# Kernel optimization log

Measured on AMD Instinct MI355X. Metric: run time of the kernel, lower is better.

The kernel has to match this reference:

```python
import jax, jax.numpy as jnp
import numpy as np

B, NQ, NKV = 4, 2048, 2048
D_MODEL, N_HEADS, D_K = 1024, 16, 64


def setup_inputs() -> dict:
    key = jax.random.key(0)
    ks = jax.random.split(key, 7)
    s = 1.0 / np.sqrt(D_MODEL)
    return {
        "x": jax.random.normal(ks[0], (B, NQ, D_MODEL), jnp.float32),
        "encoding": jax.random.normal(ks[1], (B, NKV, D_MODEL), jnp.float32),
        "position_bias": jax.random.normal(ks[2], (1, N_HEADS, NQ, NKV), jnp.float32),
        "Wq": jax.random.normal(ks[3], (D_MODEL, D_MODEL), jnp.float32) * s,
        "Wk": jax.random.normal(ks[4], (D_MODEL, D_MODEL), jnp.float32) * s,
        "Wv": jax.random.normal(ks[5], (D_MODEL, D_MODEL), jnp.float32) * s,
        "Wo": jax.random.normal(ks[6], (D_MODEL, D_MODEL), jnp.float32) * s,
    }


def _split_heads(t):
    b, n, _ = t.shape
    return t.reshape(b, n, N_HEADS, D_K).transpose(0, 2, 1, 3)


def reference(x, encoding, position_bias, Wq, Wk, Wv, Wo):
    # Projections (flax Dense, no bias): y = x @ kernel
    Q = _split_heads(x @ Wq)            # [B,H,NQ,Dk]
    K = _split_heads(encoding @ Wk)     # [B,H,NKV,Dk]
    V = _split_heads(encoding @ Wv)     # [B,H,NKV,Dk]
    # T5-style: NO 1/sqrt(d_k) scaling; additive position bias before softmax
    scores = jnp.einsum('bhqd,bhkd->bhqk', Q, K) + position_bias
    attn = jax.nn.softmax(scores, axis=-1)
    ctx = jnp.einsum('bhqk,bhkd->bhqd', attn, V)    # [B,H,NQ,Dk]
    ctx = ctx.transpose(0, 2, 1, 3).reshape(x.shape[0], x.shape[1], D_MODEL)
    return ctx @ Wo
```

## Files before the change

### kernel.cpp

```cpp
#include <hip/hip_runtime.h>

#define B_   4
#define NQ_  2048
#define NKV_ 2048
#define H_   16
#define DK_  64
#define DM_  1024
#define DKV_ 2048

typedef _Float16 f16x8 __attribute__((ext_vector_type(8)));
typedef _Float16 f16x4 __attribute__((ext_vector_type(4)));
typedef float    f32x4 __attribute__((ext_vector_type(4)));

__device__ __forceinline__ void gload_lds16(const void* g, void* l) {
  __builtin_amdgcn_global_load_lds(
      (const __attribute__((address_space(1))) unsigned int*)g,
      (__attribute__((address_space(3))) unsigned int*)l, 16, 0, 0);
}

__global__ __launch_bounds__(256) void cast_f16(const float* __restrict__ in,
                                                _Float16* __restrict__ out, int n4) {
  int i = blockIdx.x * 256 + threadIdx.x;
  if (i >= n4) return;
  float4 v = ((const float4*)in)[i];
  f16x4 o = {(_Float16)v.x, (_Float16)v.y, (_Float16)v.z, (_Float16)v.w};
  *(f16x4*)(out + (size_t)i * 4) = o;
}

__global__ __launch_bounds__(256) void wtrans(const float* __restrict__ W,
                                              _Float16* __restrict__ Wt) {
  __shared__ float tile[32][33];
  int bx = blockIdx.x & 31, by = blockIdx.x >> 5;
  int tx = threadIdx.x & 31, ty = threadIdx.x >> 5;
#pragma unroll
  for (int j = 0; j < 4; ++j)
    tile[ty + j * 8][tx] = W[(size_t)(by * 32 + ty + j * 8) * 1024 + bx * 32 + tx];
  __syncthreads();
#pragma unroll
  for (int j = 0; j < 4; ++j)
    Wt[(size_t)(bx * 32 + ty + j * 8) * 1024 + by * 32 + tx] = (_Float16)tile[tx][ty + j * 8];
}

template <int F32OUT>
__global__ __launch_bounds__(256, 2) void gemm_bt(const _Float16* __restrict__ A,
                                                  const _Float16* __restrict__ Bt,
                                                  void* __restrict__ Cp,
                                                  int M, int N, int K) {
  __shared__ _Float16 As[128 * 32];
  __shared__ _Float16 Bs[128 * 32];
  const int nbn = N >> 7;
  const int bm = blockIdx.x / nbn, bn = blockIdx.x % nbn;
  const int t = threadIdx.x, w = t >> 6, l = t & 63;
  const int lr = l & 15, lg = l >> 4;
  const int wr = w >> 1, wc = w & 1;
  const int m0 = bm << 7, n0 = bn << 7;

  f32x4 acc[4][4] = {};

  for (int k0 = 0; k0 < K; k0 += 32) {
#pragma unroll
    for (int p = 0; p < 2; ++p) {
      int off = p * 4096 + w * 1024 + l * 16;
      int row = off >> 6;
      int col = (off & 63) >> 1;
      gload_lds16(A  + (size_t)(m0 + row) * K + k0 + col, (char*)As + p * 4096 + w * 1024);
      gload_lds16(Bt + (size_t)(n0 + row) * K + k0 + col, (char*)Bs + p * 4096 + w * 1024);
    }
    __syncthreads();
    f16x8 af[4], bq[4];
#pragma unroll
    for (int i = 0; i < 4; ++i) {
      af[i] = *(const f16x8*)((const char*)As + (wr * 64 + i * 16 + lr) * 64 + lg * 16);
      bq[i] = *(const f16x8*)((const char*)Bs + (wc * 64 + i * 16 + lr) * 64 + lg * 16);
    }
#pragma unroll
    for (int i = 0; i < 4; ++i)
#pragma unroll
      for (int j = 0; j < 4; ++j)
        acc[i][j] = __builtin_amdgcn_mfma_f32_16x16x32_f16(af[i], bq[j], acc[i][j], 0, 0, 0);
    __syncthreads();
  }
#pragma unroll
  for (int i = 0; i < 4; ++i)
#pragma unroll
    for (int j = 0; j < 4; ++j)
#pragma unroll
      for (int r = 0; r < 4; ++r) {
        size_t row = m0 + wr * 64 + i * 16 + lg * 4 + r;
        size_t col = n0 + wc * 64 + j * 16 + lr;
        if (F32OUT) ((float*)Cp)[row * N + col] = acc[i][j][r];
        else ((_Float16*)Cp)[row * N + col] = (_Float16)acc[i][j][r];
      }
}

__global__ __launch_bounds__(256) void vtrans(const _Float16* __restrict__ KVb,
                                              _Float16* __restrict__ Vt) {
  __shared__ _Float16 tile[64][72];
  int idx = blockIdx.x;
  int kt = idx & 31, h = (idx >> 5) & 15, b = idx >> 9;
  int kv0 = kt << 6;
  int t = threadIdx.x;
#pragma unroll
  for (int p = 0; p < 2; ++p) {
    int c = t + p * 256;
    int row = c >> 3, cb = (c & 7) * 16;
    f16x8 v = *(const f16x8*)(KVb + (size_t)(b * NKV_ + kv0 + row) * DKV_ + 1024 + h * 64 + cb / 2);
    *(f16x8*)((char*)&tile[row][0] + cb) = v;
  }
  __syncthreads();
  int d = t & 63, j0 = (t >> 6) * 2;
#pragma unroll
  for (int jj = 0; jj < 2; ++jj) {
    int kvs = (j0 + jj) * 8;
    f16x8 o;
#pragma unroll
    for (int u = 0; u < 8; ++u) o[u] = tile[kvs + u][d];
    *(f16x8*)(Vt + ((size_t)((b * H_ + h) * 64 + d)) * NKV_ + kv0 + kvs) = o;
  }
}

__global__ __launch_bounds__(256, 4) void attn(const _Float16* __restrict__ Qb,
                                               const _Float16* __restrict__ KVb,
                                               const _Float16* __restrict__ Vt,
                                               const float* __restrict__ bias,
                                               _Float16* __restrict__ ctx) {
  __shared__ _Float16 Ks[64 * 64];
  __shared__ _Float16 Vs[64 * 64];
  __shared__ _Float16 Ps[4][16 * 64];
  const float LOG2E = 1.44269504f;
  int idx = blockIdx.x;
  int b = idx & 3, qt = (idx >> 2) & 31, h = idx >> 7;
  int t = threadIdx.x, w = t >> 6, l = t & 63, lr = l & 15, lg = l >> 4;
  int qw = (qt << 6) + (w << 4);

  const _Float16* qp = Qb + (size_t)(b * NQ_ + qw + lr) * DM_ + h * 64 + lg * 8;
  f16x8 aq0 = *(const f16x8*)qp;
  f16x8 aq1 = *(const f16x8*)(qp + 32);
#pragma unroll
  for (int u = 0; u < 8; ++u) { aq0[u] = aq0[u] * (_Float16)LOG2E; aq1[u] = aq1[u] * (_Float16)LOG2E; }

  f32x4 acc[4] = {};
  float mrow = -1e30f;
  float lsum = 0.f;

  const _Float16* Kbase = KVb + (size_t)b * NKV_ * DKV_ + h * 64;
  const _Float16* Vtb   = Vt + (size_t)(b * H_ + h) * 64 * NKV_;
  const float*    biasq = bias + ((size_t)h * NQ_ + qw + lr) * NKV_ + lg * 4;

  const int srow = t >> 3;
  const int scb  = (t & 7) * 16;

  f16x8 kreg[2], vreg[2];

  auto LOADKV = [&](int kv0) {
#pragma unroll
    for (int p = 0; p < 2; ++p) {
      int row = srow + p * 32;
      kreg[p] = *(const f16x8*)(Kbase + (size_t)(kv0 + row) * DKV_ + scb / 2);
      vreg[p] = *(const f16x8*)(Vtb + (size_t)row * NKV_ + kv0 + scb / 2);
    }
  };

  LOADKV(0);

  for (int it = 0; it < 32; ++it) {
    const int kv0 = it << 6;

#pragma unroll
    for (int p = 0; p < 2; ++p) {
      int row = srow + p * 32;
      int off = (row * 128 + scb) ^ ((row & 7) << 4);
      *(f16x8*)((char*)Ks + off) = kreg[p];
      *(f16x8*)((char*)Vs + off) = vreg[p];
    }
    __syncthreads();

    const int kvn = (it < 31) ? kv0 + 64 : kv0;
    LOADKV(kvn);

    float4 bv4[4];
#pragma unroll
    for (int nt = 0; nt < 4; ++nt)
      bv4[nt] = *(const float4*)(biasq + kv0 + nt * 16);

    f32x4 s[4];
    __builtin_amdgcn_s_setprio(1);
#pragma unroll
    for (int nt = 0; nt < 4; ++nt) {
      int row = nt * 16 + lr;
      int sw = (row & 7) << 4;
      f16x8 kf0 = *(const f16x8*)((char*)Ks + ((row * 128 + lg * 16) ^ sw));
      f16x8 kf1 = *(const f16x8*)((char*)Ks + ((row * 128 + 64 + lg * 16) ^ sw));
      f32x4 z = {0.f, 0.f, 0.f, 0.f};
      z = __builtin_amdgcn_mfma_f32_16x16x32_f16(kf0, aq0, z, 0, 0, 0);
      s[nt] = __builtin_amdgcn_mfma_f32_16x16x32_f16(kf1, aq1, z, 0, 0, 0);
    }
    __builtin_amdgcn_s_setprio(0);

#pragma unroll
    for (int nt = 0; nt < 4; ++nt) {
      s[nt][0] = fmaf(bv4[nt].x, LOG2E, s[nt][0]);
      s[nt][1] = fmaf(bv4[nt].y, LOG2E, s[nt][1]);
      s[nt][2] = fmaf(bv4[nt].z, LOG2E, s[nt][2]);
      s[nt][3] = fmaf(bv4[nt].w, LOG2E, s[nt][3]);
    }

    float pmax = fmaxf(fmaxf(s[0][0], s[0][1]), fmaxf(s[0][2], s[0][3]));
#pragma unroll
    for (int nt = 1; nt < 4; ++nt)
      pmax = fmaxf(pmax, fmaxf(fmaxf(s[nt][0], s[nt][1]), fmaxf(s[nt][2], s[nt][3])));
    pmax = fmaxf(pmax, __shfl_xor(pmax, 16));
    pmax = fmaxf(pmax, __shfl_xor(pmax, 32));

    if (__any(pmax > mrow + 8.0f)) {
      float mn = fmaxf(mrow, pmax);
      float corr = exp2f(mrow - mn);
      mrow = mn;
      lsum *= corr;
#pragma unroll
      for (int nt = 0; nt < 4; ++nt)
#pragma unroll
        for (int r = 0; r < 4; ++r) acc[nt][r] *= corr;
    }

    float rs = 0.f;
#pragma unroll
    for (int nt = 0; nt < 4; ++nt)
#pragma unroll
      for (int r = 0; r < 4; ++r) {
        float p = exp2f(s[nt][r] - mrow);
        s[nt][r] = p;
        rs += p;
      }
    rs += __shfl_xor(rs, 16);
    rs += __shfl_xor(rs, 32);
    lsum += rs;

#pragma unroll
    for (int nt = 0; nt < 4; ++nt) {
      f16x4 pk = {(_Float16)s[nt][0], (_Float16)s[nt][1],
                  (_Float16)s[nt][2], (_Float16)s[nt][3]};
      int off = (lr * 128 + nt * 32 + lg * 8) ^ ((lr & 7) << 4);
      *(f16x4*)((char*)Ps[w] + off) = pk;
    }

    __builtin_amdgcn_s_setprio(1);
#pragma unroll
    for (int kk = 0; kk < 2; ++kk) {
      f16x8 pb = *(const f16x8*)((char*)Ps[w] +
                 ((lr * 128 + kk * 64 + lg * 16) ^ ((lr & 7) << 4)));
#pragma unroll
      for (int nt = 0; nt < 4; ++nt) {
        int row = nt * 16 + lr;
        f16x8 vf = *(const f16x8*)((char*)Vs +
                 ((row * 128 + kk * 64 + lg * 16) ^ ((row & 7) << 4)));
        acc[nt] = __builtin_amdgcn_mfma_f32_16x16x32_f16(vf, pb, acc[nt], 0, 0, 0);
      }
    }
    __builtin_amdgcn_s_setprio(0);
    __syncthreads();
  }

  float inv = 1.0f / lsum;
#pragma unroll
  for (int nt = 0; nt < 4; ++nt) {
    f16x4 o = {(_Float16)(acc[nt][0] * inv), (_Float16)(acc[nt][1] * inv),
               (_Float16)(acc[nt][2] * inv), (_Float16)(acc[nt][3] * inv)};
    *(f16x4*)(ctx + ((size_t)b * NQ_ + qw + lr) * DM_ + h * 64 + nt * 16 + lg * 4) = o;
  }
}

extern "C" void kernel_launch(void* const* d_in, const int* in_sizes, int n_in,
                              void* d_out, int out_size, void* d_ws, size_t ws_size,
                              hipStream_t stream) {
  const float* x    = (const float*)d_in[0];
  const float* enc  = (const float*)d_in[1];
  const float* bias = (const float*)d_in[2];
  const float* Wq   = (const float*)d_in[3];
  const float* Wk   = (const float*)d_in[4];
  const float* Wv   = (const float*)d_in[5];
  const float* Wo   = (const float*)d_in[6];
  char* ws = (char*)d_ws;
  const size_t MiB = 1024 * 1024;
  _Float16* WqT   = (_Float16*)(ws + 0 * MiB);
  _Float16* WkT   = (_Float16*)(ws + 2 * MiB);
  _Float16* WvT   = (_Float16*)(ws + 4 * MiB);
  _Float16* WoT   = (_Float16*)(ws + 6 * MiB);
  _Float16* xf    = (_Float16*)(ws + 8 * MiB);
  _Float16* encf  = (_Float16*)(ws + 24 * MiB);
  _Float16* Qb    = (_Float16*)(ws + 40 * MiB);
  _Float16* KVb   = (_Float16*)(ws + 56 * MiB);
  _Float16* Vt    = (_Float16*)(ws + 88 * MiB);
  _Float16* ctxf  = (_Float16*)(ws + 104 * MiB);

  wtrans<<<1024, 256, 0, stream>>>(Wq, WqT);
  wtrans<<<1024, 256, 0, stream>>>(Wk, WkT);
  wtrans<<<1024, 256, 0, stream>>>(Wv, WvT);
  wtrans<<<1024, 256, 0, stream>>>(Wo, WoT);
  cast_f16<<<8192, 256, 0, stream>>>(x, xf, 2097152);
  cast_f16<<<8192, 256, 0, stream>>>(enc, encf, 2097152);
  gemm_bt<0><<<512, 256, 0, stream>>>(xf, WqT, Qb, 8192, 1024, 1024);
  gemm_bt<0><<<1024, 256, 0, stream>>>(encf, WkT, KVb, 8192, 2048, 1024);
  vtrans<<<2048, 256, 0, stream>>>(KVb, Vt);
  attn<<<2048, 256, 0, stream>>>(Qb, KVb, Vt, bias, ctxf);
  gemm_bt<1><<<512, 256, 0, stream>>>(ctxf, WoT, d_out, 8192, 1024, 1024);
}
```

Before: 353.1 us.

## Switch attention to 32x32x16 MFMA with register-resident P via permlane swaps

The attention kernel moves from 16x16x32 to 32x32x16 MFMA tiles. Each wave now handles 32 query rows instead of 16, so each block covers 128 queries and the grid is halved. The softmax probabilities are packed to f16 and rearranged in registers with permlane32_swap, which replaces the round trip through the per-wave LDS P buffer. The aim is to reuse each K/V tile across twice as many queries and to cut LDS traffic. In exchange, register pressure per wave rises and the smaller grid gives fewer blocks to spread across the GPU.

```diff
diff --git a/kernel.cpp b/kernel.cpp
--- a/kernel.cpp
+++ b/kernel.cpp
@@ -10,7 +10,11 @@
 
 typedef _Float16 f16x8 __attribute__((ext_vector_type(8)));
 typedef _Float16 f16x4 __attribute__((ext_vector_type(4)));
+typedef _Float16 f16x2 __attribute__((ext_vector_type(2)));
 typedef float    f32x4 __attribute__((ext_vector_type(4)));
+typedef float    f32x16 __attribute__((ext_vector_type(16)));
+typedef unsigned u32x2 __attribute__((ext_vector_type(2)));
+typedef unsigned u32x4 __attribute__((ext_vector_type(4)));
 
 __device__ __forceinline__ void gload_lds16(const void* g, void* l) {
   __builtin_amdgcn_global_load_lds(
@@ -119,6 +123,12 @@
   }
 }
 
+__device__ __forceinline__ void plswap(unsigned& a, unsigned& b) {
+  u32x2 r = __builtin_amdgcn_permlane32_swap(a, b, false, false);
+  a = r[0];
+  b = r[1];
+}
+
 __global__ __launch_bounds__(256, 4) void attn(const _Float16* __restrict__ Qb,
                                                const _Float16* __restrict__ KVb,
                                                const _Float16* __restrict__ Vt,
@@ -126,26 +136,30 @@
                                                _Float16* __restrict__ ctx) {
   __shared__ _Float16 Ks[64 * 64];
   __shared__ _Float16 Vs[64 * 64];
-  __shared__ _Float16 Ps[4][16 * 64];
   const float LOG2E = 1.44269504f;
   int idx = blockIdx.x;
-  int b = idx & 3, qt = (idx >> 2) & 31, h = idx >> 7;
-  int t = threadIdx.x, w = t >> 6, l = t & 63, lr = l & 15, lg = l >> 4;
-  int qw = (qt << 6) + (w << 4);
-
-  const _Float16* qp = Qb + (size_t)(b * NQ_ + qw + lr) * DM_ + h * 64 + lg * 8;
-  f16x8 aq0 = *(const f16x8*)qp;
-  f16x8 aq1 = *(const f16x8*)(qp + 32);
-#pragma unroll
-  for (int u = 0; u < 8; ++u) { aq0[u] = aq0[u] * (_Float16)LOG2E; aq1[u] = aq1[u] * (_Float16)LOG2E; }
-
-  f32x4 acc[4] = {};
-  float mrow = -1e30f;
-  float lsum = 0.f;
-
-  const _Float16* Kbase = KVb + (size_t)b * NKV_ * DKV_ + h * 64;
-  const _Float16* Vtb   = Vt + (size_t)(b * H_ + h) * 64 * NKV_;
-  const float*    biasq = bias + ((size_t)h * NQ_ + qw + lr) * NKV_ + lg * 4;
+  int b = idx & 3, qt = (idx >> 2) & 15, hd = idx >> 6;
+  int t = threadIdx.x, w = t >> 6, l = t & 63;
+  int lq = l & 31, h = l >> 5;
+  int qw = (qt << 7) + (w << 5);
+
+  f16x8 qf[4];
+  {
+    const _Float16* qp = Qb + ((size_t)(b * NQ_ + qw + lq)) * DM_ + hd * 64 + h * 8;
+#pragma unroll
+    for (int ks = 0; ks < 4; ++ks) {
+      qf[ks] = *(const f16x8*)(qp + ks * 16);
+#pragma unroll
+      for (int u = 0; u < 8; ++u) qf[ks][u] = qf[ks][u] * (_Float16)LOG2E;
+    }
+  }
+
+  f32x16 acc[2] = {};
+  float mrow = -1e30f, lsum = 0.f;
+
+  const _Float16* Kbase = KVb + (size_t)b * NKV_ * DKV_ + hd * 64;
+  const _Float16* Vtb   = Vt + (size_t)(b * H_ + hd) * 64 * NKV_;
+  const float*    biasrow = bias + ((size_t)hd * NQ_ + qw + lq) * NKV_ + 4 * h;
 
   const int srow = t >> 3;
   const int scb  = (t & 7) * 16;
@@ -175,99 +189,98 @@
     }
     __syncthreads();
 
-    const int kvn = (it < 31) ? kv0 + 64 : kv0;
-    LOADKV(kvn);
-
-    float4 bv4[4];
-#pragma unroll
-    for (int nt = 0; nt < 4; ++nt)
-      bv4[nt] = *(const float4*)(biasq + kv0 + nt * 16);
-
-    f32x4 s[4];
-    __builtin_amdgcn_s_setprio(1);
-#pragma unroll
-    for (int nt = 0; nt < 4; ++nt) {
-      int row = nt * 16 + lr;
-      int sw = (row & 7) << 4;
-      f16x8 kf0 = *(const f16x8*)((char*)Ks + ((row * 128 + lg * 16) ^ sw));
-      f16x8 kf1 = *(const f16x8*)((char*)Ks + ((row * 128 + 64 + lg * 16) ^ sw));
-      f32x4 z = {0.f, 0.f, 0.f, 0.f};
-      z = __builtin_amdgcn_mfma_f32_16x16x32_f16(kf0, aq0, z, 0, 0, 0);
-      s[nt] = __builtin_amdgcn_mfma_f32_16x16x32_f16(kf1, aq1, z, 0, 0, 0);
-    }
-    __builtin_amdgcn_s_setprio(0);
-
-#pragma unroll
-    for (int nt = 0; nt < 4; ++nt) {
-      s[nt][0] = fmaf(bv4[nt].x, LOG2E, s[nt][0]);
-      s[nt][1] = fmaf(bv4[nt].y, LOG2E, s[nt][1]);
-      s[nt][2] = fmaf(bv4[nt].z, LOG2E, s[nt][2]);
-      s[nt][3] = fmaf(bv4[nt].w, LOG2E, s[nt][3]);
-    }
-
-    float pmax = fmaxf(fmaxf(s[0][0], s[0][1]), fmaxf(s[0][2], s[0][3]));
-#pragma unroll
-    for (int nt = 1; nt < 4; ++nt)
-      pmax = fmaxf(pmax, fmaxf(fmaxf(s[nt][0], s[nt][1]), fmaxf(s[nt][2], s[nt][3])));
-    pmax = fmaxf(pmax, __shfl_xor(pmax, 16));
-    pmax = fmaxf(pmax, __shfl_xor(pmax, 32));
-
-    if (__any(pmax > mrow + 8.0f)) {
-      float mn = fmaxf(mrow, pmax);
-      float corr = exp2f(mrow - mn);
-      mrow = mn;
-      lsum *= corr;
-#pragma unroll
-      for (int nt = 0; nt < 4; ++nt)
-#pragma unroll
-        for (int r = 0; r < 4; ++r) acc[nt][r] *= corr;
-    }
-
-    float rs = 0.f;
-#pragma unroll
-    for (int nt = 0; nt < 4; ++nt)
-#pragma unroll
-      for (int r = 0; r < 4; ++r) {
-        float p = exp2f(s[nt][r] - mrow);
-        s[nt][r] = p;
+    LOADKV((it < 31) ? kv0 + 64 : kv0);
+
+#pragma unroll
+    for (int T = 0; T < 2; ++T) {
+      const float* bp = biasrow + kv0 + 32 * T;
+      float4 bv[4];
+#pragma unroll
+      for (int g = 0; g < 4; ++g) bv[g] = *(const float4*)(bp + 8 * g);
+
+      f32x16 s = {};
+      const int krow = 32 * T + lq;
+      const int ksw = (krow & 7) << 4;
+      __builtin_amdgcn_s_setprio(1);
+#pragma unroll
+      for (int ks = 0; ks < 4; ++ks) {
+        f16x8 kf = *(const f16x8*)((char*)Ks + ((krow * 128 + ks * 32 + h * 16) ^ ksw));
+        s = __builtin_amdgcn_mfma_f32_32x32x16_f16(kf, qf[ks], s, 0, 0, 0);
+      }
+      __builtin_amdgcn_s_setprio(0);
+
+#pragma unroll
+      for (int g = 0; g < 4; ++g) {
+        s[4 * g + 0] = fmaf(bv[g].x, LOG2E, s[4 * g + 0]);
+        s[4 * g + 1] = fmaf(bv[g].y, LOG2E, s[4 * g + 1]);
+        s[4 * g + 2] = fmaf(bv[g].z, LOG2E, s[4 * g + 2]);
+        s[4 * g + 3] = fmaf(bv[g].w, LOG2E, s[4 * g + 3]);
+      }
+
+      float pmax = s[0];
+#pragma unroll
+      for (int r = 1; r < 16; ++r) pmax = fmaxf(pmax, s[r]);
+      pmax = fmaxf(pmax, __shfl_xor(pmax, 32));
+
+      if (__any(pmax > mrow + 8.0f)) {
+        float mn = fmaxf(mrow, pmax);
+        float corr = exp2f(mrow - mn);
+        mrow = mn;
+        lsum *= corr;
+#pragma unroll
+        for (int r = 0; r < 16; ++r) { acc[0][r] *= corr; acc[1][r] *= corr; }
+      }
+
+      float rs = 0.f;
+#pragma unroll
+      for (int r = 0; r < 16; ++r) {
+        float p = exp2f(s[r] - mrow);
+        s[r] = p;
         rs += p;
       }
-    rs += __shfl_xor(rs, 16);
-    rs += __shfl_xor(rs, 32);
-    lsum += rs;
-
-#pragma unroll
-    for (int nt = 0; nt < 4; ++nt) {
-      f16x4 pk = {(_Float16)s[nt][0], (_Float16)s[nt][1],
-                  (_Float16)s[nt][2], (_Float16)s[nt][3]};
-      int off = (lr * 128 + nt * 32 + lg * 8) ^ ((lr & 7) << 4);
-      *(f16x4*)((char*)Ps[w] + off) = pk;
-    }
-
-    __builtin_amdgcn_s_setprio(1);
-#pragma unroll
-    for (int kk = 0; kk < 2; ++kk) {
-      f16x8 pb = *(const f16x8*)((char*)Ps[w] +
-                 ((lr * 128 + kk * 64 + lg * 16) ^ ((lr & 7) << 4)));
-#pragma unroll
-      for (int nt = 0; nt < 4; ++nt) {
-        int row = nt * 16 + lr;
-        f16x8 vf = *(const f16x8*)((char*)Vs +
-                 ((row * 128 + kk * 64 + lg * 16) ^ ((row & 7) << 4)));
-        acc[nt] = __builtin_amdgcn_mfma_f32_16x16x32_f16(vf, pb, acc[nt], 0, 0, 0);
-      }
-    }
-    __builtin_amdgcn_s_setprio(0);
+      rs += __shfl_xor(rs, 32);
+      lsum += rs;
+
+      unsigned dw[4][2];
+#pragma unroll
+      for (int g = 0; g < 4; ++g)
+#pragma unroll
+        for (int j = 0; j < 2; ++j)
+          dw[g][j] = __builtin_bit_cast(unsigned,
+              __builtin_amdgcn_cvt_pkrtz(s[4 * g + 2 * j], s[4 * g + 2 * j + 1]));
+
+      __builtin_amdgcn_s_setprio(1);
+#pragma unroll
+      for (int kp = 0; kp < 2; ++kp) {
+        unsigned A0 = dw[2 * kp][0], B0 = dw[2 * kp + 1][0];
+        unsigned A1 = dw[2 * kp][1], B1 = dw[2 * kp + 1][1];
+        plswap(A0, B0);
+        plswap(A1, B1);
+        u32x4 pv4 = {A0, A1, B0, B1};
+        f16x8 pf = __builtin_bit_cast(f16x8, pv4);
+        const int kvs = (2 * T + kp) * 32 + h * 16;
+#pragma unroll
+        for (int dt = 0; dt < 2; ++dt) {
+          int vrow = 32 * dt + lq;
+          f16x8 vf = *(const f16x8*)((char*)Vs + ((vrow * 128 + kvs) ^ ((vrow & 7) << 4)));
+          acc[dt] = __builtin_amdgcn_mfma_f32_32x32x16_f16(vf, pf, acc[dt], 0, 0, 0);
+        }
+      }
+      __builtin_amdgcn_s_setprio(0);
+    }
     __syncthreads();
   }
 
   float inv = 1.0f / lsum;
-#pragma unroll
-  for (int nt = 0; nt < 4; ++nt) {
-    f16x4 o = {(_Float16)(acc[nt][0] * inv), (_Float16)(acc[nt][1] * inv),
-               (_Float16)(acc[nt][2] * inv), (_Float16)(acc[nt][3] * inv)};
-    *(f16x4*)(ctx + ((size_t)b * NQ_ + qw + lr) * DM_ + h * 64 + nt * 16 + lg * 4) = o;
-  }
+  _Float16* cp = ctx + ((size_t)b * NQ_ + qw + lq) * DM_ + hd * 64 + 4 * h;
+#pragma unroll
+  for (int dt = 0; dt < 2; ++dt)
+#pragma unroll
+    for (int g = 0; g < 4; ++g) {
+      f16x4 o = {(_Float16)(acc[dt][4 * g + 0] * inv), (_Float16)(acc[dt][4 * g + 1] * inv),
+                 (_Float16)(acc[dt][4 * g + 2] * inv), (_Float16)(acc[dt][4 * g + 3] * inv)};
+      *(f16x4*)(cp + 32 * dt + 8 * g) = o;
+    }
 }
 
 extern "C" void kernel_launch(void* const* d_in, const int* in_sizes, int n_in,
@@ -302,6 +315,6 @@
   gemm_bt<0><<<512, 256, 0, stream>>>(xf, WqT, Qb, 8192, 1024, 1024);
   gemm_bt<0><<<1024, 256, 0, stream>>>(encf, WkT, KVb, 8192, 2048, 1024);
   vtrans<<<2048, 256, 0, stream>>>(KVb, Vt);
-  attn<<<2048, 256, 0, stream>>>(Qb, KVb, Vt, bias, ctxf);
+  attn<<<1024, 256, 0, stream>>>(Qb, KVb, Vt, bias, ctxf);
   gemm_bt<1><<<512, 256, 0, stream>>>(ctxf, WoT, d_out, 8192, 1024, 1024);
 }
```

Result: slower. 378.7 us (+7.3%).

## Stage 128-wide KV tiles per sync and remap block indices for L2 locality

Applied to the files above, without the earlier changes.

The attention kernel now stages 128 KV rows per iteration, split into two 64-wide softmax sub-steps, which halves the number of barriers and global-to-LDS rounds. The V tile layout and swizzle change to a 256-byte row stride to match. Block indices are also remapped so that eight consecutive blocks share the same batch and neighbouring head/query-tile pairs, aiming to improve cache reuse of K/V across concurrently running blocks. LDS usage doubles for K and V and more registers hold prefetched tiles, which may lower occupancy.

```diff
diff --git a/kernel.cpp b/kernel.cpp
--- a/kernel.cpp
+++ b/kernel.cpp
@@ -124,16 +124,19 @@
                                                const _Float16* __restrict__ Vt,
                                                const float* __restrict__ bias,
                                                _Float16* __restrict__ ctx) {
-  __shared__ _Float16 Ks[64 * 64];
-  __shared__ _Float16 Vs[64 * 64];
+  __shared__ _Float16 Ks[128 * 64];
+  __shared__ _Float16 Vs[64 * 128];
   __shared__ _Float16 Ps[4][16 * 64];
   const float LOG2E = 1.44269504f;
   int idx = blockIdx.x;
-  int b = idx & 3, qt = (idx >> 2) & 31, h = idx >> 7;
+  int xr = idx & 7, m = idx >> 3;
+  int b = m & 3;
+  int hq = (m >> 2) * 8 + xr;
+  int hd = hq >> 5, qt = hq & 31;
   int t = threadIdx.x, w = t >> 6, l = t & 63, lr = l & 15, lg = l >> 4;
   int qw = (qt << 6) + (w << 4);
 
-  const _Float16* qp = Qb + (size_t)(b * NQ_ + qw + lr) * DM_ + h * 64 + lg * 8;
+  const _Float16* qp = Qb + (size_t)(b * NQ_ + qw + lr) * DM_ + hd * 64 + lg * 8;
   f16x8 aq0 = *(const f16x8*)qp;
   f16x8 aq1 = *(const f16x8*)(qp + 32);
 #pragma unroll
@@ -143,121 +146,124 @@
   float mrow = -1e30f;
   float lsum = 0.f;
 
-  const _Float16* Kbase = KVb + (size_t)b * NKV_ * DKV_ + h * 64;
-  const _Float16* Vtb   = Vt + (size_t)(b * H_ + h) * 64 * NKV_;
-  const float*    biasq = bias + ((size_t)h * NQ_ + qw + lr) * NKV_ + lg * 4;
-
-  const int srow = t >> 3;
-  const int scb  = (t & 7) * 16;
-
-  f16x8 kreg[2], vreg[2];
+  const _Float16* Kbase = KVb + (size_t)b * NKV_ * DKV_ + hd * 64;
+  const _Float16* Vtb   = Vt + (size_t)(b * H_ + hd) * 64 * NKV_;
+  const float*    biasq = bias + ((size_t)hd * NQ_ + qw + lr) * NKV_ + lg * 4;
+
+  const int ksrow = t >> 3, kscb = (t & 7) * 16;
+  const int vsrow = t >> 4, vscb = (t & 15) * 16;
+
+  f16x8 kreg[4], vreg[4];
 
   auto LOADKV = [&](int kv0) {
 #pragma unroll
-    for (int p = 0; p < 2; ++p) {
-      int row = srow + p * 32;
-      kreg[p] = *(const f16x8*)(Kbase + (size_t)(kv0 + row) * DKV_ + scb / 2);
-      vreg[p] = *(const f16x8*)(Vtb + (size_t)row * NKV_ + kv0 + scb / 2);
+    for (int p = 0; p < 4; ++p) {
+      kreg[p] = *(const f16x8*)(Kbase + (size_t)(kv0 + ksrow + p * 32) * DKV_ + kscb / 2);
+      vreg[p] = *(const f16x8*)(Vtb + (size_t)(vsrow + p * 16) * NKV_ + kv0 + vscb / 2);
     }
   };
 
   LOADKV(0);
 
-  for (int it = 0; it < 32; ++it) {
-    const int kv0 = it << 6;
-
-#pragma unroll
-    for (int p = 0; p < 2; ++p) {
-      int row = srow + p * 32;
-      int off = (row * 128 + scb) ^ ((row & 7) << 4);
-      *(f16x8*)((char*)Ks + off) = kreg[p];
-      *(f16x8*)((char*)Vs + off) = vreg[p];
+  for (int it = 0; it < 16; ++it) {
+    const int kv0 = it << 7;
+
+#pragma unroll
+    for (int p = 0; p < 4; ++p) {
+      int krow = ksrow + p * 32;
+      *(f16x8*)((char*)Ks + ((krow * 128 + kscb) ^ ((krow & 7) << 4))) = kreg[p];
+      int vrow = vsrow + p * 16;
+      *(f16x8*)((char*)Vs + ((vrow * 256 + vscb) ^ ((vrow & 15) << 4))) = vreg[p];
     }
     __syncthreads();
 
-    const int kvn = (it < 31) ? kv0 + 64 : kv0;
-    LOADKV(kvn);
-
-    float4 bv4[4];
-#pragma unroll
-    for (int nt = 0; nt < 4; ++nt)
-      bv4[nt] = *(const float4*)(biasq + kv0 + nt * 16);
-
-    f32x4 s[4];
-    __builtin_amdgcn_s_setprio(1);
-#pragma unroll
-    for (int nt = 0; nt < 4; ++nt) {
-      int row = nt * 16 + lr;
-      int sw = (row & 7) << 4;
-      f16x8 kf0 = *(const f16x8*)((char*)Ks + ((row * 128 + lg * 16) ^ sw));
-      f16x8 kf1 = *(const f16x8*)((char*)Ks + ((row * 128 + 64 + lg * 16) ^ sw));
-      f32x4 z = {0.f, 0.f, 0.f, 0.f};
-      z = __builtin_amdgcn_mfma_f32_16x16x32_f16(kf0, aq0, z, 0, 0, 0);
-      s[nt] = __builtin_amdgcn_mfma_f32_16x16x32_f16(kf1, aq1, z, 0, 0, 0);
-    }
-    __builtin_amdgcn_s_setprio(0);
-
-#pragma unroll
-    for (int nt = 0; nt < 4; ++nt) {
-      s[nt][0] = fmaf(bv4[nt].x, LOG2E, s[nt][0]);
-      s[nt][1] = fmaf(bv4[nt].y, LOG2E, s[nt][1]);
-      s[nt][2] = fmaf(bv4[nt].z, LOG2E, s[nt][2]);
-      s[nt][3] = fmaf(bv4[nt].w, LOG2E, s[nt][3]);
-    }
-
-    float pmax = fmaxf(fmaxf(s[0][0], s[0][1]), fmaxf(s[0][2], s[0][3]));
-#pragma unroll
-    for (int nt = 1; nt < 4; ++nt)
-      pmax = fmaxf(pmax, fmaxf(fmaxf(s[nt][0], s[nt][1]), fmaxf(s[nt][2], s[nt][3])));
-    pmax = fmaxf(pmax, __shfl_xor(pmax, 16));
-    pmax = fmaxf(pmax, __shfl_xor(pmax, 32));
-
-    if (__any(pmax > mrow + 8.0f)) {
-      float mn = fmaxf(mrow, pmax);
-      float corr = exp2f(mrow - mn);
-      mrow = mn;
-      lsum *= corr;
+    LOADKV((it < 15) ? kv0 + 128 : kv0);
+
+#pragma unroll
+    for (int T = 0; T < 2; ++T) {
+      const int kvh = kv0 + 64 * T;
+
+      float4 bv4[4];
 #pragma unroll
       for (int nt = 0; nt < 4; ++nt)
-#pragma unroll
-        for (int r = 0; r < 4; ++r) acc[nt][r] *= corr;
-    }
-
-    float rs = 0.f;
-#pragma unroll
-    for (int nt = 0; nt < 4; ++nt)
-#pragma unroll
-      for (int r = 0; r < 4; ++r) {
-        float p = exp2f(s[nt][r] - mrow);
-        s[nt][r] = p;
-        rs += p;
-      }
-    rs += __shfl_xor(rs, 16);
-    rs += __shfl_xor(rs, 32);
-    lsum += rs;
-
-#pragma unroll
-    for (int nt = 0; nt < 4; ++nt) {
-      f16x4 pk = {(_Float16)s[nt][0], (_Float16)s[nt][1],
-                  (_Float16)s[nt][2], (_Float16)s[nt][3]};
-      int off = (lr * 128 + nt * 32 + lg * 8) ^ ((lr & 7) << 4);
-      *(f16x4*)((char*)Ps[w] + off) = pk;
-    }
-
-    __builtin_amdgcn_s_setprio(1);
-#pragma unroll
-    for (int kk = 0; kk < 2; ++kk) {
-      f16x8 pb = *(const f16x8*)((char*)Ps[w] +
-                 ((lr * 128 + kk * 64 + lg * 16) ^ ((lr & 7) << 4)));
+        bv4[nt] = *(const float4*)(biasq + kvh + nt * 16);
+
+      f32x4 s[4];
+      __builtin_amdgcn_s_setprio(1);
 #pragma unroll
       for (int nt = 0; nt < 4; ++nt) {
-        int row = nt * 16 + lr;
-        f16x8 vf = *(const f16x8*)((char*)Vs +
-                 ((row * 128 + kk * 64 + lg * 16) ^ ((row & 7) << 4)));
-        acc[nt] = __builtin_amdgcn_mfma_f32_16x16x32_f16(vf, pb, acc[nt], 0, 0, 0);
-      }
-    }
-    __builtin_amdgcn_s_setprio(0);
+        int row = T * 64 + nt * 16 + lr;
+        int sw = (row & 7) << 4;
+        f16x8 kf0 = *(const f16x8*)((char*)Ks + ((row * 128 + lg * 16) ^ sw));
+        f16x8 kf1 = *(const f16x8*)((char*)Ks + ((row * 128 + 64 + lg * 16) ^ sw));
+        f32x4 z = {0.f, 0.f, 0.f, 0.f};
+        z = __builtin_amdgcn_mfma_f32_16x16x32_f16(kf0, aq0, z, 0, 0, 0);
+        s[nt] = __builtin_amdgcn_mfma_f32_16x16x32_f16(kf1, aq1, z, 0, 0, 0);
+      }
+      __builtin_amdgcn_s_setprio(0);
+
+#pragma unroll
+      for (int nt = 0; nt < 4; ++nt) {
+        s[nt][0] = fmaf(bv4[nt].x, LOG2E, s[nt][0]);
+        s[nt][1] = fmaf(bv4[nt].y, LOG2E, s[nt][1]);
+        s[nt][2] = fmaf(bv4[nt].z, LOG2E, s[nt][2]);
+        s[nt][3] = fmaf(bv4[nt].w, LOG2E, s[nt][3]);
+      }
+
+      float pmax = fmaxf(fmaxf(s[0][0], s[0][1]), fmaxf(s[0][2], s[0][3]));
+#pragma unroll
+      for (int nt = 1; nt < 4; ++nt)
+        pmax = fmaxf(pmax, fmaxf(fmaxf(s[nt][0], s[nt][1]), fmaxf(s[nt][2], s[nt][3])));
+      pmax = fmaxf(pmax, __shfl_xor(pmax, 16));
+      pmax = fmaxf(pmax, __shfl_xor(pmax, 32));
+
+      if (__any(pmax > mrow + 8.0f)) {
+        float mn = fmaxf(mrow, pmax);
+        float corr = exp2f(mrow - mn);
+        mrow = mn;
+        lsum *= corr;
+#pragma unroll
+        for (int nt = 0; nt < 4; ++nt)
+#pragma unroll
+          for (int r = 0; r < 4; ++r) acc[nt][r] *= corr;
+      }
+
+      float rs = 0.f;
+#pragma unroll
+      for (int nt = 0; nt < 4; ++nt)
+#pragma unroll
+        for (int r = 0; r < 4; ++r) {
+          float p = exp2f(s[nt][r] - mrow);
+          s[nt][r] = p;
+          rs += p;
+        }
+      rs += __shfl_xor(rs, 16);
+      rs += __shfl_xor(rs, 32);
+      lsum += rs;
+
+#pragma unroll
+      for (int nt = 0; nt < 4; ++nt) {
+        f16x4 pk = {(_Float16)s[nt][0], (_Float16)s[nt][1],
+                    (_Float16)s[nt][2], (_Float16)s[nt][3]};
+        int off = (lr * 128 + nt * 32 + lg * 8) ^ ((lr & 7) << 4);
+        *(f16x4*)((char*)Ps[w] + off) = pk;
+      }
+
+      __builtin_amdgcn_s_setprio(1);
+#pragma unroll
+      for (int kk = 0; kk < 2; ++kk) {
+        f16x8 pb = *(const f16x8*)((char*)Ps[w] +
+                   ((lr * 128 + kk * 64 + lg * 16) ^ ((lr & 7) << 4)));
+#pragma unroll
+        for (int nt = 0; nt < 4; ++nt) {
+          int vrow = nt * 16 + lr;
+          f16x8 vf = *(const f16x8*)((char*)Vs +
+                   ((vrow * 256 + T * 128 + kk * 64 + lg * 16) ^ ((vrow & 15) << 4)));
+          acc[nt] = __builtin_amdgcn_mfma_f32_16x16x32_f16(vf, pb, acc[nt], 0, 0, 0);
+        }
+      }
+      __builtin_amdgcn_s_setprio(0);
+    }
     __syncthreads();
   }
 
@@ -266,7 +272,7 @@
   for (int nt = 0; nt < 4; ++nt) {
     f16x4 o = {(_Float16)(acc[nt][0] * inv), (_Float16)(acc[nt][1] * inv),
                (_Float16)(acc[nt][2] * inv), (_Float16)(acc[nt][3] * inv)};
-    *(f16x4*)(ctx + ((size_t)b * NQ_ + qw + lr) * DM_ + h * 64 + nt * 16 + lg * 4) = o;
+    *(f16x4*)(ctx + ((size_t)b * NQ_ + qw + lr) * DM_ + hd * 64 + nt * 16 + lg * 4) = o;
   }
 }
 
```

After: 543.3 us. 1.54x slower.

## Process 32 query rows per wave in attention to reuse K/V tiles

Applied to the files above, without the earlier changes.

Each wave in the attention kernel now handles two 16-row query subtiles (128 queries per block), so each K and V fragment loaded from LDS feeds twice as many MFMAs. The grid is halved to match. The next K/V prefetch is also moved after the QK MFMAs, and the second bias load is issued after that prefetch. This cuts K/V global and LDS traffic per query, at the cost of more registers (two accumulator sets and two Q fragments) and a larger P buffer in LDS, which could lower occupancy. The grid also drops to 1024 blocks.

```diff
diff --git a/kernel.cpp b/kernel.cpp
--- a/kernel.cpp
+++ b/kernel.cpp
@@ -126,26 +126,33 @@
                                                _Float16* __restrict__ ctx) {
   __shared__ _Float16 Ks[64 * 64];
   __shared__ _Float16 Vs[64 * 64];
-  __shared__ _Float16 Ps[4][16 * 64];
+  __shared__ _Float16 Ps[4][32 * 64];
   const float LOG2E = 1.44269504f;
   int idx = blockIdx.x;
-  int b = idx & 3, qt = (idx >> 2) & 31, h = idx >> 7;
+  int b = idx & 3, qt = (idx >> 2) & 15, hd = idx >> 6;
   int t = threadIdx.x, w = t >> 6, l = t & 63, lr = l & 15, lg = l >> 4;
-  int qw = (qt << 6) + (w << 4);
-
-  const _Float16* qp = Qb + (size_t)(b * NQ_ + qw + lr) * DM_ + h * 64 + lg * 8;
-  f16x8 aq0 = *(const f16x8*)qp;
-  f16x8 aq1 = *(const f16x8*)(qp + 32);
-#pragma unroll
-  for (int u = 0; u < 8; ++u) { aq0[u] = aq0[u] * (_Float16)LOG2E; aq1[u] = aq1[u] * (_Float16)LOG2E; }
-
-  f32x4 acc[4] = {};
-  float mrow = -1e30f;
-  float lsum = 0.f;
-
-  const _Float16* Kbase = KVb + (size_t)b * NKV_ * DKV_ + h * 64;
-  const _Float16* Vtb   = Vt + (size_t)(b * H_ + h) * 64 * NKV_;
-  const float*    biasq = bias + ((size_t)h * NQ_ + qw + lr) * NKV_ + lg * 4;
+  int qw = (qt << 7) + (w << 5);
+
+  f16x8 aq[2][2];
+#pragma unroll
+  for (int qe = 0; qe < 2; ++qe) {
+    const _Float16* qp = Qb + (size_t)(b * NQ_ + qw + qe * 16 + lr) * DM_ + hd * 64 + lg * 8;
+    aq[qe][0] = *(const f16x8*)qp;
+    aq[qe][1] = *(const f16x8*)(qp + 32);
+#pragma unroll
+    for (int u = 0; u < 8; ++u) {
+      aq[qe][0][u] = aq[qe][0][u] * (_Float16)LOG2E;
+      aq[qe][1][u] = aq[qe][1][u] * (_Float16)LOG2E;
+    }
+  }
+
+  f32x4 acc[2][4] = {};
+  float mrow[2] = {-1e30f, -1e30f};
+  float lsum[2] = {0.f, 0.f};
+
+  const _Float16* Kbase = KVb + (size_t)b * NKV_ * DKV_ + hd * 64;
+  const _Float16* Vtb   = Vt + (size_t)(b * H_ + hd) * 64 * NKV_;
+  const float*    biasq = bias + ((size_t)hd * NQ_ + qw + lr) * NKV_ + lg * 4;
 
   const int srow = t >> 3;
   const int scb  = (t & 7) * 16;
@@ -175,15 +182,12 @@
     }
     __syncthreads();
 
-    const int kvn = (it < 31) ? kv0 + 64 : kv0;
-    LOADKV(kvn);
-
-    float4 bv4[4];
+    float4 bv0[4];
 #pragma unroll
     for (int nt = 0; nt < 4; ++nt)
-      bv4[nt] = *(const float4*)(biasq + kv0 + nt * 16);
-
-    f32x4 s[4];
+      bv0[nt] = *(const float4*)(biasq + kv0 + nt * 16);
+
+    f32x4 s[2][4];
     __builtin_amdgcn_s_setprio(1);
 #pragma unroll
     for (int nt = 0; nt < 4; ++nt) {
@@ -191,82 +195,108 @@
       int sw = (row & 7) << 4;
       f16x8 kf0 = *(const f16x8*)((char*)Ks + ((row * 128 + lg * 16) ^ sw));
       f16x8 kf1 = *(const f16x8*)((char*)Ks + ((row * 128 + 64 + lg * 16) ^ sw));
-      f32x4 z = {0.f, 0.f, 0.f, 0.f};
-      z = __builtin_amdgcn_mfma_f32_16x16x32_f16(kf0, aq0, z, 0, 0, 0);
-      s[nt] = __builtin_amdgcn_mfma_f32_16x16x32_f16(kf1, aq1, z, 0, 0, 0);
+#pragma unroll
+      for (int qe = 0; qe < 2; ++qe) {
+        f32x4 z = {0.f, 0.f, 0.f, 0.f};
+        z = __builtin_amdgcn_mfma_f32_16x16x32_f16(kf0, aq[qe][0], z, 0, 0, 0);
+        s[qe][nt] = __builtin_amdgcn_mfma_f32_16x16x32_f16(kf1, aq[qe][1], z, 0, 0, 0);
+      }
     }
     __builtin_amdgcn_s_setprio(0);
 
-#pragma unroll
-    for (int nt = 0; nt < 4; ++nt) {
-      s[nt][0] = fmaf(bv4[nt].x, LOG2E, s[nt][0]);
-      s[nt][1] = fmaf(bv4[nt].y, LOG2E, s[nt][1]);
-      s[nt][2] = fmaf(bv4[nt].z, LOG2E, s[nt][2]);
-      s[nt][3] = fmaf(bv4[nt].w, LOG2E, s[nt][3]);
-    }
-
-    float pmax = fmaxf(fmaxf(s[0][0], s[0][1]), fmaxf(s[0][2], s[0][3]));
-#pragma unroll
-    for (int nt = 1; nt < 4; ++nt)
-      pmax = fmaxf(pmax, fmaxf(fmaxf(s[nt][0], s[nt][1]), fmaxf(s[nt][2], s[nt][3])));
-    pmax = fmaxf(pmax, __shfl_xor(pmax, 16));
-    pmax = fmaxf(pmax, __shfl_xor(pmax, 32));
-
-    if (__any(pmax > mrow + 8.0f)) {
-      float mn = fmaxf(mrow, pmax);
-      float corr = exp2f(mrow - mn);
-      mrow = mn;
-      lsum *= corr;
+    LOADKV((it < 31) ? kv0 + 64 : kv0);
+
+    float4 bv1[4];
+#pragma unroll
+    for (int nt = 0; nt < 4; ++nt)
+      bv1[nt] = *(const float4*)(biasq + 16 * NKV_ + kv0 + nt * 16);
+
+#pragma unroll
+    for (int qe = 0; qe < 2; ++qe) {
+      float4* bv = qe ? bv1 : bv0;
+#pragma unroll
+      for (int nt = 0; nt < 4; ++nt) {
+        s[qe][nt][0] = fmaf(bv[nt].x, LOG2E, s[qe][nt][0]);
+        s[qe][nt][1] = fmaf(bv[nt].y, LOG2E, s[qe][nt][1]);
+        s[qe][nt][2] = fmaf(bv[nt].z, LOG2E, s[qe][nt][2]);
+        s[qe][nt][3] = fmaf(bv[nt].w, LOG2E, s[qe][nt][3]);
+      }
+
+      float pmax = fmaxf(fmaxf(s[qe][0][0], s[qe][0][1]), fmaxf(s[qe][0][2], s[qe][0][3]));
+#pragma unroll
+      for (int nt = 1; nt < 4; ++nt)
+        pmax = fmaxf(pmax, fmaxf(fmaxf(s[qe][nt][0], s[qe][nt][1]),
+                                 fmaxf(s[qe][nt][2], s[qe][nt][3])));
+      pmax = fmaxf(pmax, __shfl_xor(pmax, 16));
+      pmax = fmaxf(pmax, __shfl_xor(pmax, 32));
+
+      if (__any(pmax > mrow[qe] + 8.0f)) {
+        float mn = fmaxf(mrow[qe], pmax);
+        float corr = exp2f(mrow[qe] - mn);
+        mrow[qe] = mn;
+        lsum[qe] *= corr;
+#pragma unroll
+        for (int nt = 0; nt < 4; ++nt)
+#pragma unroll
+          for (int r = 0; r < 4; ++r) acc[qe][nt][r] *= corr;
+      }
+
+      float rs = 0.f;
 #pragma unroll
       for (int nt = 0; nt < 4; ++nt)
 #pragma unroll
-        for (int r = 0; r < 4; ++r) acc[nt][r] *= corr;
-    }
-
-    float rs = 0.f;
-#pragma unroll
-    for (int nt = 0; nt < 4; ++nt)
-#pragma unroll
-      for (int r = 0; r < 4; ++r) {
-        float p = exp2f(s[nt][r] - mrow);
-        s[nt][r] = p;
-        rs += p;
-      }
-    rs += __shfl_xor(rs, 16);
-    rs += __shfl_xor(rs, 32);
-    lsum += rs;
-
-#pragma unroll
-    for (int nt = 0; nt < 4; ++nt) {
-      f16x4 pk = {(_Float16)s[nt][0], (_Float16)s[nt][1],
-                  (_Float16)s[nt][2], (_Float16)s[nt][3]};
-      int off = (lr * 128 + nt * 32 + lg * 8) ^ ((lr & 7) << 4);
-      *(f16x4*)((char*)Ps[w] + off) = pk;
+        for (int r = 0; r < 4; ++r) {
+          float p = exp2f(s[qe][nt][r] - mrow[qe]);
+          s[qe][nt][r] = p;
+          rs += p;
+        }
+      rs += __shfl_xor(rs, 16);
+      rs += __shfl_xor(rs, 32);
+      lsum[qe] += rs;
+
+      const int prow = qe * 16 + lr;
+#pragma unroll
+      for (int nt = 0; nt < 4; ++nt) {
+        f16x4 pk = {(_Float16)s[qe][nt][0], (_Float16)s[qe][nt][1],
+                    (_Float16)s[qe][nt][2], (_Float16)s[qe][nt][3]};
+        int off = (prow * 128 + nt * 32 + lg * 8) ^ ((lr & 7) << 4);
+        *(f16x4*)((char*)Ps[w] + off) = pk;
+      }
     }
 
     __builtin_amdgcn_s_setprio(1);
 #pragma unroll
     for (int kk = 0; kk < 2; ++kk) {
-      f16x8 pb = *(const f16x8*)((char*)Ps[w] +
-                 ((lr * 128 + kk * 64 + lg * 16) ^ ((lr & 7) << 4)));
+      f16x8 pb[2];
+#pragma unroll
+      for (int qe = 0; qe < 2; ++qe) {
+        int prow = qe * 16 + lr;
+        pb[qe] = *(const f16x8*)((char*)Ps[w] +
+                 ((prow * 128 + kk * 64 + lg * 16) ^ ((lr & 7) << 4)));
+      }
 #pragma unroll
       for (int nt = 0; nt < 4; ++nt) {
-        int row = nt * 16 + lr;
+        int vrow = nt * 16 + lr;
         f16x8 vf = *(const f16x8*)((char*)Vs +
-                 ((row * 128 + kk * 64 + lg * 16) ^ ((row & 7) << 4)));
-        acc[nt] = __builtin_amdgcn_mfma_f32_16x16x32_f16(vf, pb, acc[nt], 0, 0, 0);
+                 ((vrow * 128 + kk * 64 + lg * 16) ^ ((vrow & 7) << 4)));
+#pragma unroll
+        for (int qe = 0; qe < 2; ++qe)
+          acc[qe][nt] = __builtin_amdgcn_mfma_f32_16x16x32_f16(vf, pb[qe], acc[qe][nt], 0, 0, 0);
       }
     }
     __builtin_amdgcn_s_setprio(0);
     __syncthreads();
   }
 
-  float inv = 1.0f / lsum;
-#pragma unroll
-  for (int nt = 0; nt < 4; ++nt) {
-    f16x4 o = {(_Float16)(acc[nt][0] * inv), (_Float16)(acc[nt][1] * inv),
-               (_Float16)(acc[nt][2] * inv), (_Float16)(acc[nt][3] * inv)};
-    *(f16x4*)(ctx + ((size_t)b * NQ_ + qw + lr) * DM_ + h * 64 + nt * 16 + lg * 4) = o;
+#pragma unroll
+  for (int qe = 0; qe < 2; ++qe) {
+    float inv = 1.0f / lsum[qe];
+#pragma unroll
+    for (int nt = 0; nt < 4; ++nt) {
+      f16x4 o = {(_Float16)(acc[qe][nt][0] * inv), (_Float16)(acc[qe][nt][1] * inv),
+                 (_Float16)(acc[qe][nt][2] * inv), (_Float16)(acc[qe][nt][3] * inv)};
+      *(f16x4*)(ctx + ((size_t)b * NQ_ + qw + qe * 16 + lr) * DM_ + hd * 64 + nt * 16 + lg * 4) = o;
+    }
   }
 }
 
@@ -302,6 +332,6 @@
   gemm_bt<0><<<512, 256, 0, stream>>>(xf, WqT, Qb, 8192, 1024, 1024);
   gemm_bt<0><<<1024, 256, 0, stream>>>(encf, WkT, KVb, 8192, 2048, 1024);
   vtrans<<<2048, 256, 0, stream>>>(KVb, Vt);
-  attn<<<2048, 256, 0, stream>>>(Qb, KVb, Vt, bias, ctxf);
+  attn<<<1024, 256, 0, stream>>>(Qb, KVb, Vt, bias, ctxf);
   gemm_bt<1><<<512, 256, 0, stream>>>(ctxf, WoT, d_out, 8192, 1024, 1024);
 }
```

Result: slower. 517.9 us (+46.7%).
